# Optimization experiments

Hardware: AMD Instinct MI355X
Metric: run time of the kernel (lower is better)

## Reference

```python
import jax, jax.numpy as jnp
import numpy as np

N, F, E = 10000, 128, 640000
HID_RO = 64


def setup_inputs() -> dict:
    key = jax.random.key(0)
    ks = jax.random.split(key, 16)
    s = 1.0 / np.sqrt(F)
    inp = {
        'h': jax.random.normal(ks[0], (N, F), jnp.float32),
        'src_idx': jax.random.randint(ks[1], (E,), 0, N, jnp.int32),
        'dst_idx': jax.random.randint(ks[2], (E,), 0, N, jnp.int32),
        # message-creation MLP (F -> F -> F)
        'W1': jax.random.normal(ks[3], (F, F), jnp.float32) * s,
        'b1': jnp.zeros((F,), jnp.float32),
        'W2': jax.random.normal(ks[4], (F, F), jnp.float32) * s,
        'b2': jnp.zeros((F,), jnp.float32),
        # attention aggregation kernels
        'node_kernel': jax.random.normal(ks[5], (F, F), jnp.float32) * s,
        'attn_kernel': jax.random.normal(ks[6], (2 * F, 1), jnp.float32) * s,
        # feed-forward update (agg + h -> new h)
        'Wu': jax.random.normal(ks[7], (2 * F, F), jnp.float32) * s,
        'bu': jnp.zeros((F,), jnp.float32),
        # readout MLP (F -> 64 -> 1)
        'Wr1': jax.random.normal(ks[8], (F, HID_RO), jnp.float32) * s,
        'br1': jnp.zeros((HID_RO,), jnp.float32),
        'Wr2': jax.random.normal(ks[9], (HID_RO, 1), jnp.float32) * (1.0 / np.sqrt(HID_RO)),
        'br2': jnp.zeros((1,), jnp.float32),
    }
    return inp


def reference(h, src_idx, dst_idx, W1, b1, W2, b2, node_kernel, attn_kernel,
              Wu, bu, Wr1, br1, Wr2, br2):
    n = h.shape[0]
    # per-edge gather + message-creation NN  [E, F]
    h_src = h[src_idx]
    m = jax.nn.relu(h_src @ W1 + b1) @ W2 + b2
    # attention aggregation (GAT-style): transform messages, score vs dst state
    wh = m @ node_kernel                      # [E, F]
    h_dst = h[dst_idx]                        # [E, F]
    e = jax.nn.leaky_relu(jnp.concatenate([wh, h_dst], axis=-1) @ attn_kernel,
                          negative_slope=0.2)[:, 0]  # [E]
    # per-destination segment softmax (numerically stable)
    e_max = jax.ops.segment_max(e, dst_idx, num_segments=n)
    ex = jnp.exp(e - e_max[dst_idx])
    denom = jax.ops.segment_sum(ex, dst_idx, num_segments=n)
    alpha = ex / (denom[dst_idx] + 1e-9)
    # scatter-reduce weighted messages into destination states  [N, F]
    agg = jax.ops.segment_sum(m * alpha[:, None], dst_idx, num_segments=n)
    # feed-forward update
    h_new = jax.nn.relu(jnp.concatenate([agg, h], axis=-1) @ Wu + bu)
    # readout MLP -> per-node scalar
    out = jax.nn.relu(h_new @ Wr1 + br1) @ Wr2 + br2  # [N, 1]
    return out
```

## Files before the change

### kernel.cpp

```cpp
#include <hip/hip_runtime.h>
#include <hip/hip_bf16.h>
#include <hip/hip_fp16.h>

#define F 128
#define HID 64
#define KMAX 4
#define DEG_CAP 256
#define NTM 16
#define NTU 16
#define CHUNK_LOG 13
#define CHUNK (1 << CHUNK_LOG)


__global__ __launch_bounds__(256) void fused_front(
    const int* __restrict__ dst, unsigned short* __restrict__ cnt,
    unsigned short* __restrict__ rank,
    int e, int n, int histBlocks,
    const float* __restrict__ h,
    const float* __restrict__ W1, const float* __restrict__ b1,
    const float* __restrict__ W2, const float* __restrict__ b2,
    const float* __restrict__ nk, const float* __restrict__ attn,
    __half* __restrict__ Mh, float* __restrict__ p, float* __restrict__ q)
{
    __shared__ __align__(16) int lhist[10240];
    int tid = threadIdx.x;

    if ((int)blockIdx.x < histBlocks) {
        int n4 = n >> 2;
        int4* lh4 = (int4*)lhist;
        for (int i = tid; i < n4; i += 256) lh4[i] = make_int4(0, 0, 0, 0);
        for (int i = (n4 << 2) + tid; i < n; i += 256) lhist[i] = 0;
        __syncthreads();

        int base = (int)blockIdx.x << CHUNK_LOG;
        int lim = min(e - base, CHUNK);
        int lim4 = lim >> 2;
        const int4* d4 = (const int4*)(dst + base);
        for (int k = tid; k < lim4; k += 256) {
            int4 dv = d4[k];
            ushort4 rv;
            rv.x = (unsigned short)atomicAdd(&lhist[dv.x], 1);
            rv.y = (unsigned short)atomicAdd(&lhist[dv.y], 1);
            rv.z = (unsigned short)atomicAdd(&lhist[dv.z], 1);
            rv.w = (unsigned short)atomicAdd(&lhist[dv.w], 1);
            *(ushort4*)&rank[base + 4 * k] = rv;
        }
        for (int k = (lim4 << 2) + tid; k < lim; k += 256)
            rank[base + k] = (unsigned short)atomicAdd(&lhist[dst[base + k]], 1);
        __syncthreads();

        unsigned int* crow = (unsigned int*)(cnt + (size_t)blockIdx.x * n);
        int nh = n >> 1;
        for (int i = tid; i < nh; i += 256) {
            unsigned int v = ((unsigned int)lhist[2 * i] & 0xffffu) |
                             ((unsigned int)lhist[2 * i + 1] << 16);
            crow[i] = v;
        }
        return;
    }

    float (*hsTs)[F] = (float (*)[F])lhist;
    float (*Wc)[F]   = (float (*)[F])((char*)lhist + 8192);
    float* v1s       = (float*)((char*)lhist + 24576);

    int bm = blockIdx.x - histBlocks;
    int row0 = bm * NTM;
    int j0 = (tid & 31) * 4;
    int r0 = (tid >> 5) * 2;

    #pragma unroll
    for (int it = 0; it < 2; ++it) {
        int s4 = tid + it * 256;
        int r = s4 >> 5, c4 = s4 & 31;
        int row = row0 + r;
        float4 v = make_float4(0, 0, 0, 0);
        if (row < n) v = *(const float4*)&h[(size_t)row * F + c4 * 4];
        *(float4*)&hsTs[r][c4 * 4] = v;
    }
    if (tid < F) {
        float a = 0.f;
        const float4* nkr = (const float4*)&nk[(size_t)tid * F];
        const float4* at4 = (const float4*)attn;
        #pragma unroll 8
        for (int j = 0; j < 32; ++j) {
            float4 nv = nkr[j]; float4 av = at4[j];
            a = fmaf(nv.x, av.x, a); a = fmaf(nv.y, av.y, a);
            a = fmaf(nv.z, av.z, a); a = fmaf(nv.w, av.w, a);
        }
        v1s[tid] = a;
    }
    __syncthreads();

    {
        int r = tid >> 4, kp = tid & 15;
        float qa = 0.f;
        #pragma unroll
        for (int c = 0; c < 2; ++c) {
            float4 hv = *(const float4*)&hsTs[r][kp * 8 + c * 4];
            float4 av = *(const float4*)&attn[F + kp * 8 + c * 4];
            qa = fmaf(hv.x, av.x, qa); qa = fmaf(hv.y, av.y, qa);
            qa = fmaf(hv.z, av.z, qa); qa = fmaf(hv.w, av.w, qa);
        }
        #pragma unroll
        for (int off = 1; off < 16; off <<= 1) qa += __shfl_xor(qa, off, 64);
        int row = row0 + r;
        if (kp == 0 && row < n) q[row] = qa;
    }

    float4 acc[2];
    {
        float4 bv = *(const float4*)&b1[j0];
        acc[0] = bv; acc[1] = bv;
    }
    for (int cc = 0; cc < 4; ++cc) {
        int kc = ((cc + bm) & 3) * 32;
        __syncthreads();
        #pragma unroll
        for (int it = 0; it < 4; ++it) {
            int s4 = tid + it * 256;
            int wr = s4 >> 5, wc4 = s4 & 31;
            *(float4*)&Wc[wr][wc4 * 4] =
                *(const float4*)&W1[(size_t)(kc + wr) * F + wc4 * 4];
        }
        __syncthreads();
        #pragma unroll
        for (int k4 = 0; k4 < 8; ++k4) {
            int kk = k4 * 4;
            float4 a0 = *(const float4*)&hsTs[r0 + 0][kc + kk];
            float4 a1 = *(const float4*)&hsTs[r0 + 1][kc + kk];
            #pragma unroll
            for (int k = 0; k < 4; ++k) {
                float4 b = *(const float4*)&Wc[kk + k][j0];
                float av0 = k == 0 ? a0.x : k == 1 ? a0.y : k == 2 ? a0.z : a0.w;
                float av1 = k == 0 ? a1.x : k == 1 ? a1.y : k == 2 ? a1.z : a1.w;
                acc[0].x = fmaf(av0, b.x, acc[0].x); acc[0].y = fmaf(av0, b.y, acc[0].y);
                acc[0].z = fmaf(av0, b.z, acc[0].z); acc[0].w = fmaf(av0, b.w, acc[0].w);
                acc[1].x = fmaf(av1, b.x, acc[1].x); acc[1].y = fmaf(av1, b.y, acc[1].y);
                acc[1].z = fmaf(av1, b.z, acc[1].z); acc[1].w = fmaf(av1, b.w, acc[1].w);
            }
        }
    }
    __syncthreads();
    #pragma unroll
    for (int i = 0; i < 2; ++i) {
        float4 t = acc[i];
        t.x = fmaxf(t.x, 0.f); t.y = fmaxf(t.y, 0.f);
        t.z = fmaxf(t.z, 0.f); t.w = fmaxf(t.w, 0.f);
        *(float4*)&hsTs[r0 + i][j0] = t;
    }

    {
        float4 bv = *(const float4*)&b2[j0];
        acc[0] = bv; acc[1] = bv;
    }
    for (int cc = 0; cc < 4; ++cc) {
        int kc = ((cc + bm) & 3) * 32;
        __syncthreads();
        #pragma unroll
        for (int it = 0; it < 4; ++it) {
            int s4 = tid + it * 256;
            int wr = s4 >> 5, wc4 = s4 & 31;
            *(float4*)&Wc[wr][wc4 * 4] =
                *(const float4*)&W2[(size_t)(kc + wr) * F + wc4 * 4];
        }
        __syncthreads();
        #pragma unroll
        for (int k4 = 0; k4 < 8; ++k4) {
            int kk = k4 * 4;
            float4 a0 = *(const float4*)&hsTs[r0 + 0][kc + kk];
            float4 a1 = *(const float4*)&hsTs[r0 + 1][kc + kk];
            #pragma unroll
            for (int k = 0; k < 4; ++k) {
                float4 b = *(const float4*)&Wc[kk + k][j0];
                float av0 = k == 0 ? a0.x : k == 1 ? a0.y : k == 2 ? a0.z : a0.w;
                float av1 = k == 0 ? a1.x : k == 1 ? a1.y : k == 2 ? a1.z : a1.w;
                acc[0].x = fmaf(av0, b.x, acc[0].x); acc[0].y = fmaf(av0, b.y, acc[0].y);
                acc[0].z = fmaf(av0, b.z, acc[0].z); acc[0].w = fmaf(av0, b.w, acc[0].w);
                acc[1].x = fmaf(av1, b.x, acc[1].x); acc[1].y = fmaf(av1, b.y, acc[1].y);
                acc[1].z = fmaf(av1, b.z, acc[1].z); acc[1].w = fmaf(av1, b.w, acc[1].w);
            }
        }
    }

    float4 v1v = *(const float4*)&v1s[j0];
    #pragma unroll
    for (int i = 0; i < 2; ++i) {
        int row = row0 + r0 + i;
        if (row < n) {
            __half hv[4];
            hv[0] = __float2half(acc[i].x); hv[1] = __float2half(acc[i].y);
            hv[2] = __float2half(acc[i].z); hv[3] = __float2half(acc[i].w);
            *(uint2*)&Mh[(size_t)row * F + j0] = *(uint2*)hv;
        }
        float pp = acc[i].x * v1v.x + acc[i].y * v1v.y +
                   acc[i].z * v1v.z + acc[i].w * v1v.w;
        #pragma unroll
        for (int off = 1; off < 32; off <<= 1) pp += __shfl_xor(pp, off, 64);
        if ((tid & 31) == 0 && row < n) p[row] = pp;
    }
}

__global__ __launch_bounds__(256) void scan_block(
    unsigned short* __restrict__ cnt, int* __restrict__ rstart,
    int* __restrict__ bsum, int n, int hb)
{
    int tid = threadIdx.x;
    int i = blockIdx.x * 256 + tid;
    int run = 0;
    if (i < n) {
        size_t stride = (size_t)n;
        size_t idx = (size_t)i;
        int r = 0;
        for (; r + 8 <= hb; r += 8) {
            int c0 = cnt[idx];
            int c1 = cnt[idx + stride];
            int c2 = cnt[idx + 2 * stride];
            int c3 = cnt[idx + 3 * stride];
            int c4 = cnt[idx + 4 * stride];
            int c5 = cnt[idx + 5 * stride];
            int c6 = cnt[idx + 6 * stride];
            int c7 = cnt[idx + 7 * stride];
            cnt[idx]              = (unsigned short)run;
            cnt[idx + stride]     = (unsigned short)(run + c0);
            cnt[idx + 2 * stride] = (unsigned short)(run + (c0 + c1));
            cnt[idx + 3 * stride] = (unsigned short)(run + (c0 + c1 + c2));
            cnt[idx + 4 * stride] = (unsigned short)(run + (c0 + c1 + c2 + c3));
            cnt[idx + 5 * stride] = (unsigned short)(run + (c0 + c1 + c2 + c3 + c4));
            cnt[idx + 6 * stride] = (unsigned short)(run + (c0 + c1 + c2 + c3 + c4 + c5));
            cnt[idx + 7 * stride] = (unsigned short)(run + (c0 + c1 + c2 + c3 + c4 + c5 + c6));
            run += c0 + c1 + c2 + c3 + c4 + c5 + c6 + c7;
            idx += 8 * stride;
        }
        for (; r < hb; ++r) {
            int c = cnt[idx];
            cnt[idx] = (unsigned short)run;
            run += c;
            idx += stride;
        }
    }
    int v = run;
    int lane = tid & 63, wv = tid >> 6;
    int x = v;
    #pragma unroll
    for (int off = 1; off < 64; off <<= 1) {
        int t = __shfl_up(x, off, 64);
        if (lane >= off) x += t;
    }
    __shared__ int wsum[4];
    if (lane == 63) wsum[wv] = x;
    __syncthreads();
    int woff = 0;
    #pragma unroll
    for (int wdx = 0; wdx < 4; ++wdx) woff += (wdx < wv) ? wsum[wdx] : 0;
    int incl = x + woff;
    if (i < n) rstart[i] = incl - v;
    if (tid == 255) bsum[blockIdx.x] = incl;
}

__global__ __launch_bounds__(256) void fill_kernel(
    const int* __restrict__ dst, const int* __restrict__ src,
    const unsigned short* __restrict__ rank, const int* __restrict__ rstart,
    const unsigned short* __restrict__ cntoff, const int* __restrict__ bsum,
    unsigned short* __restrict__ src_sorted, int n, int nb, int e)
{
    __shared__ int sbo[64];
    int tid = threadIdx.x;
    if (tid < 64) {
        int v = (tid < nb) ? bsum[tid] : 0;
        int x = v;
        #pragma unroll
        for (int off = 1; off < 64; off <<= 1) {
            int t = __shfl_up(x, off, 64);
            if (tid >= off) x += t;
        }
        sbo[tid] = x - v;
    }
    __syncthreads();
    int i = blockIdx.x * 256 + tid;
    if (i < e) {
        int d = dst[i];
        int rep = i >> CHUNK_LOG;
        int pos = rstart[d] + sbo[d >> 8] + (int)cntoff[(size_t)rep * n + d] + (int)rank[i];
        src_sorted[pos] = (unsigned short)src[i];
    }
}

__global__ __launch_bounds__(256) void agg_softmax_gather(
    const __half* __restrict__ Mh, const float* __restrict__ p,
    const float* __restrict__ q, const int* __restrict__ rstart,
    const int* __restrict__ bsum, const unsigned short* __restrict__ src_sorted,
    float* __restrict__ agg, int n, int nb, int e)
{
    __shared__ int2 buf[4][DEG_CAP];
    __shared__ int sbo[64];
    int tid = threadIdx.x;
    if (tid < 64) {
        int v = (tid < nb) ? bsum[tid] : 0;
        int x = v;
        #pragma unroll
        for (int off = 1; off < 64; off <<= 1) {
            int t = __shfl_up(x, off, 64);
            if (tid >= off) x += t;
        }
        sbo[tid] = x - v;
    }
    __syncthreads();

    int lane = tid & 63;
    int wv   = tid >> 6;
    int node = blockIdx.x * 4 + wv;
    if (node >= n) return;

    int start = rstart[node] + sbo[node >> 8];
    int end   = (node + 1 < n) ? rstart[node + 1] + sbo[(node + 1) >> 8] : e;
    int deg   = end - start;
    float qn  = q[node];

    float w[KMAX];
    int   sidx[KMAX];
    float lmax = -1e30f;

    #pragma unroll
    for (int k = 0; k < KMAX; ++k) {
        int i = start + lane + (k << 6);
        bool valid = (i < end);
        int sv = valid ? (int)src_sorted[i] : 0;
        float pv = valid ? p[sv] : 0.0f;
        float sc = pv + qn;
        float ev = (sc > 0.0f) ? sc : 0.2f * sc;
        w[k] = valid ? ev : -1e30f;
        sidx[k] = sv;
        lmax = fmaxf(lmax, w[k]);
    }
    for (int i = start + DEG_CAP + lane; i < end; i += 64) {
        float sc = p[(int)src_sorted[i]] + qn;
        float ev = (sc > 0.0f) ? sc : 0.2f * sc;
        lmax = fmaxf(lmax, ev);
    }
    #pragma unroll
    for (int off = 32; off >= 1; off >>= 1)
        lmax = fmaxf(lmax, __shfl_xor(lmax, off, 64));

    float lsum = 0.0f;
    #pragma unroll
    for (int k = 0; k < KMAX; ++k) {
        float ex = (w[k] > -1e29f) ? __expf(w[k] - lmax) : 0.0f;
        w[k] = ex;
        lsum += ex;
    }
    for (int i = start + DEG_CAP + lane; i < end; i += 64) {
        float sc = p[(int)src_sorted[i]] + qn;
        float ev = (sc > 0.0f) ? sc : 0.2f * sc;
        lsum += __expf(ev - lmax);
    }
    #pragma unroll
    for (int off = 32; off >= 1; off >>= 1)
        lsum += __shfl_xor(lsum, off, 64);
    float inv = 1.0f / (lsum + 1e-9f);

    #pragma unroll
    for (int k = 0; k < KMAX; ++k)
        buf[wv][lane + (k << 6)] = make_int2(__float_as_int(w[k] * inv), sidx[k]);

    const uint4* M16 = (const uint4*)Mh;
    int sub16 = lane & 15;
    int quar  = lane >> 4;
    float acc[8] = {0.f, 0.f, 0.f, 0.f, 0.f, 0.f, 0.f, 0.f};
    int lim = min(deg, DEG_CAP);
    lim = (lim + 15) & ~15;

    for (int base = 0; base < lim; base += 16) {
        int2  rr[4];
        uint4 mm[4];
        #pragma unroll
        for (int u = 0; u < 4; ++u) rr[u] = buf[wv][base + quar + 4 * u];
        #pragma unroll
        for (int u = 0; u < 4; ++u) mm[u] = M16[(size_t)rr[u].y * 16 + sub16];
        #pragma unroll
        for (int u = 0; u < 4; ++u) {
            float wu = __int_as_float(rr[u].x);
            const __half2* hp = (const __half2*)&mm[u];
            float2 f0 = __half22float2(hp[0]);
            float2 f1 = __half22float2(hp[1]);
            float2 f2 = __half22float2(hp[2]);
            float2 f3 = __half22float2(hp[3]);
            acc[0] = fmaf(wu, f0.x, acc[0]); acc[1] = fmaf(wu, f0.y, acc[1]);
            acc[2] = fmaf(wu, f1.x, acc[2]); acc[3] = fmaf(wu, f1.y, acc[3]);
            acc[4] = fmaf(wu, f2.x, acc[4]); acc[5] = fmaf(wu, f2.y, acc[5]);
            acc[6] = fmaf(wu, f3.x, acc[6]); acc[7] = fmaf(wu, f3.y, acc[7]);
        }
    }

    for (int base = start + DEG_CAP; base < end; base += 64) {
        int i = base + lane;
        float ex = 0.f; int sv = 0;
        if (i < end) {
            sv = (int)src_sorted[i];
            float sc = p[sv] + qn;
            float ev = (sc > 0.0f) ? sc : 0.2f * sc;
            ex = __expf(ev - lmax) * inv;
        }
        buf[wv][lane] = make_int2(__float_as_int(ex), sv);
        for (int b2 = 0; b2 < 64; b2 += 4) {
            int2 rr = buf[wv][b2 + quar];
            uint4 mm = M16[(size_t)rr.y * 16 + sub16];
            float wu = __int_as_float(rr.x);
            const __half2* hp = (const __half2*)&mm;
            float2 f0 = __half22float2(hp[0]);
            float2 f1 = __half22float2(hp[1]);
            float2 f2 = __half22float2(hp[2]);
            float2 f3 = __half22float2(hp[3]);
            acc[0] = fmaf(wu, f0.x, acc[0]); acc[1] = fmaf(wu, f0.y, acc[1]);
            acc[2] = fmaf(wu, f1.x, acc[2]); acc[3] = fmaf(wu, f1.y, acc[3]);
            acc[4] = fmaf(wu, f2.x, acc[4]); acc[5] = fmaf(wu, f2.y, acc[5]);
            acc[6] = fmaf(wu, f3.x, acc[6]); acc[7] = fmaf(wu, f3.y, acc[7]);
        }
    }

    #pragma unroll
    for (int j = 0; j < 8; ++j) {
        acc[j] += __shfl_xor(acc[j], 16, 64);
        acc[j] += __shfl_xor(acc[j], 32, 64);
    }
    if (quar == 0) {
        float* dst0 = &agg[(size_t)node * F + sub16 * 8];
        *(float4*)dst0       = make_float4(acc[0], acc[1], acc[2], acc[3]);
        *(float4*)(dst0 + 4) = make_float4(acc[4], acc[5], acc[6], acc[7]);
    }
}

__global__ __launch_bounds__(256) void update_readout_v5(
    const float* __restrict__ agg, const float* __restrict__ h,
    const float* __restrict__ Wu, const float* __restrict__ bu,
    const float* __restrict__ Wr1, const float* __restrict__ br1,
    const float* __restrict__ Wr2, const float* __restrict__ br2,
    float* __restrict__ out, int n)
{
    __shared__ __align__(16) float smem[8192];
    float (*X)[2 * F] = (float (*)[2 * F])smem;
    int tid = threadIdx.x;
    int wv   = tid >> 6;
    int lane = tid & 63;
    int row0 = blockIdx.x * NTU;
    int j0 = (lane & 31) * 4;
    int rh = (lane >> 5) * 8;

    #pragma unroll
    for (int it = 0; it < 4; ++it) {
        int s4 = tid + it * 256;
        int r = s4 >> 6, c4 = s4 & 63;
        int row = row0 + r;
        float4 v = make_float4(0, 0, 0, 0);
        if (row < n) {
            if (c4 < 32) v = *(const float4*)&agg[(size_t)row * F + c4 * 4];
            else         v = *(const float4*)&h[(size_t)row * F + (c4 - 32) * 4];
        }
        *(float4*)&X[r][c4 * 4] = v;
    }
    __syncthreads();

    float4 acc[8];
    #pragma unroll
    for (int i = 0; i < 8; ++i) acc[i] = make_float4(0.f, 0.f, 0.f, 0.f);
    int kbase = wv * 64;
    for (int k4 = 0; k4 < 16; ++k4) {
        int kk = kbase + k4 * 4;
        float4 a[8];
        #pragma unroll
        for (int r = 0; r < 8; ++r) a[r] = *(const float4*)&X[rh + r][kk];
        #pragma unroll
        for (int k = 0; k < 4; ++k) {
            float4 b = *(const float4*)&Wu[(size_t)(kk + k) * F + j0];
            #pragma unroll
            for (int r = 0; r < 8; ++r) {
                float av = k == 0 ? a[r].x : k == 1 ? a[r].y : k == 2 ? a[r].z : a[r].w;
                acc[r].x = fmaf(av, b.x, acc[r].x);
                acc[r].y = fmaf(av, b.y, acc[r].y);
                acc[r].z = fmaf(av, b.z, acc[r].z);
                acc[r].w = fmaf(av, b.w, acc[r].w);
            }
        }
    }
    __syncthreads();

    #pragma unroll
    for (int r = 0; r < 8; ++r)
        *(float4*)&smem[wv * 2048 + (rh + r) * 128 + j0] = acc[r];
    __syncthreads();

    #pragma unroll
    for (int u = 0; u < 2; ++u) {
        int idx = tid * 2 + u;
        int row = idx >> 5, c4 = (idx & 31) * 4;
        float4 s0 = *(const float4*)&smem[0 * 2048 + row * 128 + c4];
        float4 s1 = *(const float4*)&smem[1 * 2048 + row * 128 + c4];
        float4 s2 = *(const float4*)&smem[2 * 2048 + row * 128 + c4];
        float4 s3 = *(const float4*)&smem[3 * 2048 + row * 128 + c4];
        float4 bv = *(const float4*)&bu[c4];
        float4 t;
        t.x = fmaxf(s0.x + s1.x + s2.x + s3.x + bv.x, 0.f);
        t.y = fmaxf(s0.y + s1.y + s2.y + s3.y + bv.y, 0.f);
        t.z = fmaxf(s0.z + s1.z + s2.z + s3.z + bv.z, 0.f);
        t.w = fmaxf(s0.w + s1.w + s2.w + s3.w + bv.w, 0.f);
        *(float4*)&smem[row * 128 + c4] = t;
    }
    __syncthreads();

    int h0 = (lane & 31) * 2;
    float r1a[8], r1b[8];
    #pragma unroll
    for (int r = 0; r < 8; ++r) { r1a[r] = 0.f; r1b[r] = 0.f; }
    int kb2 = wv * 32;
    for (int k4 = 0; k4 < 8; ++k4) {
        int kk = kb2 + k4 * 4;
        float4 a[8];
        #pragma unroll
        for (int r = 0; r < 8; ++r) a[r] = *(const float4*)&smem[(rh + r) * 128 + kk];
        #pragma unroll
        for (int k = 0; k < 4; ++k) {
            float2 b = *(const float2*)&Wr1[(size_t)(kk + k) * HID + h0];
            #pragma unroll
            for (int r = 0; r < 8; ++r) {
                float av = k == 0 ? a[r].x : k == 1 ? a[r].y : k == 2 ? a[r].z : a[r].w;
                r1a[r] = fmaf(av, b.x, r1a[r]);
                r1b[r] = fmaf(av, b.y, r1b[r]);
            }
        }
    }
    #pragma unroll
    for (int r = 0; r < 8; ++r) {
        smem[2048 + wv * 1024 + (rh + r) * 64 + h0]     = r1a[r];
        smem[2048 + wv * 1024 + (rh + r) * 64 + h0 + 1] = r1b[r];
    }
    __syncthreads();

    {
        int row = tid >> 4;
        int hp  = (tid & 15) * 4;
        float val = 0.f;
        #pragma unroll
        for (int j = 0; j < 4; ++j) {
            int hh = hp + j;
            float s = br1[hh]
                    + smem[2048 + 0 * 1024 + row * 64 + hh]
                    + smem[2048 + 1 * 1024 + row * 64 + hh]
                    + smem[2048 + 2 * 1024 + row * 64 + hh]
                    + smem[2048 + 3 * 1024 + row * 64 + hh];
            val = fmaf(fmaxf(s, 0.f), Wr2[hh], val);
        }
        #pragma unroll
        for (int off = 1; off < 16; off <<= 1) val += __shfl_xor(val, off, 64);
        int orow = row0 + row;
        if ((tid & 15) == 0 && orow < n) out[orow] = val + br2[0];
    }
}

extern "C" void kernel_launch(void* const* d_in, const int* in_sizes, int n_in,
                              void* d_out, int out_size, void* d_ws, size_t ws_size,
                              hipStream_t stream) {
    const float* h    = (const float*)d_in[0];
    const int*   src  = (const int*)d_in[1];
    const int*   dst  = (const int*)d_in[2];
    const float* W1   = (const float*)d_in[3];
    const float* b1   = (const float*)d_in[4];
    const float* W2   = (const float*)d_in[5];
    const float* b2   = (const float*)d_in[6];
    const float* nk   = (const float*)d_in[7];
    const float* attn = (const float*)d_in[8];
    const float* Wu   = (const float*)d_in[9];
    const float* bu   = (const float*)d_in[10];
    const float* Wr1  = (const float*)d_in[11];
    const float* br1  = (const float*)d_in[12];
    const float* Wr2  = (const float*)d_in[13];
    const float* br2  = (const float*)d_in[14];
    float* out = (float*)d_out;

    int n = in_sizes[0] / F;
    int e = in_sizes[1];
    int nb = (n + 255) / 256;
    int hb = (e + CHUNK - 1) >> CHUNK_LOG;
    int mlpBlocks  = (n + NTM - 1) / NTM;
    int updBlocks  = (n + NTU - 1) / NTU;
    int fillBlocks = (e + 255) / 256;

    char* ws = (char*)d_ws;
    size_t off = 0;
    auto alloc = [&](size_t bytes) {
        void* pp = ws + off;
        off += (bytes + 511) & ~(size_t)511;
        return pp;
    };
    __half* Mh             = (__half*)alloc((size_t)n * F * 2);
    float* aggws           = (float*)alloc((size_t)n * F * 4);
    float* p               = (float*)alloc((size_t)n * 4);
    float* q               = (float*)alloc((size_t)n * 4);
    unsigned short* cnt    = (unsigned short*)alloc((size_t)hb * n * 2);
    int*   rstart          = (int*)alloc((size_t)(n + 1) * 4);
    int*   bsum            = (int*)alloc((size_t)(nb + 1) * 4);
    unsigned short* rank   = (unsigned short*)alloc((size_t)e * 2);
    unsigned short* srcsort= (unsigned short*)alloc((size_t)e * 2);

    fused_front<<<hb + mlpBlocks, 256, 0, stream>>>(
        dst, cnt, rank, e, n, hb,
        h, W1, b1, W2, b2, nk, attn, Mh, p, q);
    scan_block<<<nb, 256, 0, stream>>>(cnt, rstart, bsum, n, hb);
    fill_kernel<<<fillBlocks, 256, 0, stream>>>(dst, src, rank, rstart,
                                                cnt, bsum, srcsort,
                                                n, nb, e);
    agg_softmax_gather<<<(n + 3) / 4, 256, 0, stream>>>(Mh, p, q, rstart, bsum,
                                                        srcsort, aggws, n, nb, e);
    update_readout_v5<<<updBlocks, 256, 0, stream>>>(aggws, h, Wu, bu,
                                                     Wr1, br1, Wr2, br2,
                                                     out, n);
}
```

Measured before the change: 156.6 us.

## Fuse softmax-gather aggregation into update/readout kernel via shared memory

Merges the per-node softmax aggregation kernel into the update/readout kernel. Each block now handles 16 nodes, with each wave aggregating 4 nodes in turn and writing the result straight into the shared-memory X tile. This removes the global agg buffer round trip and one kernel launch. In exchange the grid shrinks from about 2500 to 625 blocks and each wave processes its nodes serially, which may reduce latency hiding for the gather.

```diff
diff --git a/kernel.cpp b/kernel.cpp
--- a/kernel.cpp
+++ b/kernel.cpp
@@ -285,180 +285,174 @@
     }
 }
 
-__global__ __launch_bounds__(256) void agg_softmax_gather(
+__global__ __launch_bounds__(256) void agg_update(
     const __half* __restrict__ Mh, const float* __restrict__ p,
     const float* __restrict__ q, const int* __restrict__ rstart,
     const int* __restrict__ bsum, const unsigned short* __restrict__ src_sorted,
-    float* __restrict__ agg, int n, int nb, int e)
-{
-    __shared__ int2 buf[4][DEG_CAP];
-    __shared__ int sbo[64];
-    int tid = threadIdx.x;
-    if (tid < 64) {
-        int v = (tid < nb) ? bsum[tid] : 0;
-        int x = v;
-        #pragma unroll
-        for (int off = 1; off < 64; off <<= 1) {
-            int t = __shfl_up(x, off, 64);
-            if (tid >= off) x += t;
-        }
-        sbo[tid] = x - v;
-    }
-    __syncthreads();
-
-    int lane = tid & 63;
-    int wv   = tid >> 6;
-    int node = blockIdx.x * 4 + wv;
-    if (node >= n) return;
-
-    int start = rstart[node] + sbo[node >> 8];
-    int end   = (node + 1 < n) ? rstart[node + 1] + sbo[(node + 1) >> 8] : e;
-    int deg   = end - start;
-    float qn  = q[node];
-
-    float w[KMAX];
-    int   sidx[KMAX];
-    float lmax = -1e30f;
-
-    #pragma unroll
-    for (int k = 0; k < KMAX; ++k) {
-        int i = start + lane + (k << 6);
-        bool valid = (i < end);
-        int sv = valid ? (int)src_sorted[i] : 0;
-        float pv = valid ? p[sv] : 0.0f;
-        float sc = pv + qn;
-        float ev = (sc > 0.0f) ? sc : 0.2f * sc;
-        w[k] = valid ? ev : -1e30f;
-        sidx[k] = sv;
-        lmax = fmaxf(lmax, w[k]);
-    }
-    for (int i = start + DEG_CAP + lane; i < end; i += 64) {
-        float sc = p[(int)src_sorted[i]] + qn;
-        float ev = (sc > 0.0f) ? sc : 0.2f * sc;
-        lmax = fmaxf(lmax, ev);
-    }
-    #pragma unroll
-    for (int off = 32; off >= 1; off >>= 1)
-        lmax = fmaxf(lmax, __shfl_xor(lmax, off, 64));
-
-    float lsum = 0.0f;
-    #pragma unroll
-    for (int k = 0; k < KMAX; ++k) {
-        float ex = (w[k] > -1e29f) ? __expf(w[k] - lmax) : 0.0f;
-        w[k] = ex;
-        lsum += ex;
-    }
-    for (int i = start + DEG_CAP + lane; i < end; i += 64) {
-        float sc = p[(int)src_sorted[i]] + qn;
-        float ev = (sc > 0.0f) ? sc : 0.2f * sc;
-        lsum += __expf(ev - lmax);
-    }
-    #pragma unroll
-    for (int off = 32; off >= 1; off >>= 1)
-        lsum += __shfl_xor(lsum, off, 64);
-    float inv = 1.0f / (lsum + 1e-9f);
-
-    #pragma unroll
-    for (int k = 0; k < KMAX; ++k)
-        buf[wv][lane + (k << 6)] = make_int2(__float_as_int(w[k] * inv), sidx[k]);
-
-    const uint4* M16 = (const uint4*)Mh;
-    int sub16 = lane & 15;
-    int quar  = lane >> 4;
-    float acc[8] = {0.f, 0.f, 0.f, 0.f, 0.f, 0.f, 0.f, 0.f};
-    int lim = min(deg, DEG_CAP);
-    lim = (lim + 15) & ~15;
-
-    for (int base = 0; base < lim; base += 16) {
-        int2  rr[4];
-        uint4 mm[4];
-        #pragma unroll
-        for (int u = 0; u < 4; ++u) rr[u] = buf[wv][base + quar + 4 * u];
-        #pragma unroll
-        for (int u = 0; u < 4; ++u) mm[u] = M16[(size_t)rr[u].y * 16 + sub16];
-        #pragma unroll
-        for (int u = 0; u < 4; ++u) {
-            float wu = __int_as_float(rr[u].x);
-            const __half2* hp = (const __half2*)&mm[u];
-            float2 f0 = __half22float2(hp[0]);
-            float2 f1 = __half22float2(hp[1]);
-            float2 f2 = __half22float2(hp[2]);
-            float2 f3 = __half22float2(hp[3]);
-            acc[0] = fmaf(wu, f0.x, acc[0]); acc[1] = fmaf(wu, f0.y, acc[1]);
-            acc[2] = fmaf(wu, f1.x, acc[2]); acc[3] = fmaf(wu, f1.y, acc[3]);
-            acc[4] = fmaf(wu, f2.x, acc[4]); acc[5] = fmaf(wu, f2.y, acc[5]);
-            acc[6] = fmaf(wu, f3.x, acc[6]); acc[7] = fmaf(wu, f3.y, acc[7]);
-        }
-    }
-
-    for (int base = start + DEG_CAP; base < end; base += 64) {
-        int i = base + lane;
-        float ex = 0.f; int sv = 0;
-        if (i < end) {
-            sv = (int)src_sorted[i];
-            float sc = p[sv] + qn;
-            float ev = (sc > 0.0f) ? sc : 0.2f * sc;
-            ex = __expf(ev - lmax) * inv;
-        }
-        buf[wv][lane] = make_int2(__float_as_int(ex), sv);
-        for (int b2 = 0; b2 < 64; b2 += 4) {
-            int2 rr = buf[wv][b2 + quar];
-            uint4 mm = M16[(size_t)rr.y * 16 + sub16];
-            float wu = __int_as_float(rr.x);
-            const __half2* hp = (const __half2*)&mm;
-            float2 f0 = __half22float2(hp[0]);
-            float2 f1 = __half22float2(hp[1]);
-            float2 f2 = __half22float2(hp[2]);
-            float2 f3 = __half22float2(hp[3]);
-            acc[0] = fmaf(wu, f0.x, acc[0]); acc[1] = fmaf(wu, f0.y, acc[1]);
-            acc[2] = fmaf(wu, f1.x, acc[2]); acc[3] = fmaf(wu, f1.y, acc[3]);
-            acc[4] = fmaf(wu, f2.x, acc[4]); acc[5] = fmaf(wu, f2.y, acc[5]);
-            acc[6] = fmaf(wu, f3.x, acc[6]); acc[7] = fmaf(wu, f3.y, acc[7]);
-        }
-    }
-
-    #pragma unroll
-    for (int j = 0; j < 8; ++j) {
-        acc[j] += __shfl_xor(acc[j], 16, 64);
-        acc[j] += __shfl_xor(acc[j], 32, 64);
-    }
-    if (quar == 0) {
-        float* dst0 = &agg[(size_t)node * F + sub16 * 8];
-        *(float4*)dst0       = make_float4(acc[0], acc[1], acc[2], acc[3]);
-        *(float4*)(dst0 + 4) = make_float4(acc[4], acc[5], acc[6], acc[7]);
-    }
-}
-
-__global__ __launch_bounds__(256) void update_readout_v5(
-    const float* __restrict__ agg, const float* __restrict__ h,
+    const float* __restrict__ h,
     const float* __restrict__ Wu, const float* __restrict__ bu,
     const float* __restrict__ Wr1, const float* __restrict__ br1,
     const float* __restrict__ Wr2, const float* __restrict__ br2,
-    float* __restrict__ out, int n)
+    float* __restrict__ out, int n, int nb, int e)
 {
     __shared__ __align__(16) float smem[8192];
     float (*X)[2 * F] = (float (*)[2 * F])smem;
+    int2* bufa = (int2*)&smem[4096];
+    int*  sbo  = (int*)&smem[6144];
+
     int tid = threadIdx.x;
     int wv   = tid >> 6;
     int lane = tid & 63;
     int row0 = blockIdx.x * NTU;
+
+    if (tid < 64) {
+        int v = (tid < nb) ? bsum[tid] : 0;
+        int x = v;
+        #pragma unroll
+        for (int off = 1; off < 64; off <<= 1) {
+            int t = __shfl_up(x, off, 64);
+            if (tid >= off) x += t;
+        }
+        sbo[tid] = x - v;
+    }
+    #pragma unroll
+    for (int it = 0; it < 2; ++it) {
+        int s4 = tid + it * 256;
+        int r = s4 >> 5, c4 = s4 & 31;
+        int row = row0 + r;
+        float4 v = make_float4(0, 0, 0, 0);
+        if (row < n) v = *(const float4*)&h[(size_t)row * F + c4 * 4];
+        *(float4*)&X[r][128 + c4 * 4] = v;
+    }
+    __syncthreads();
+
+    const uint4* M16 = (const uint4*)Mh;
+    int sub16 = lane & 15;
+    int quar  = lane >> 4;
+    int2* bufw = bufa + wv * DEG_CAP;
+
+    for (int s = 0; s < 4; ++s) {
+        int lr = wv * 4 + s;
+        int node = row0 + lr;
+        if (node >= n) break;
+
+        int start = rstart[node] + sbo[node >> 8];
+        int end   = (node + 1 < n) ? rstart[node + 1] + sbo[(node + 1) >> 8] : e;
+        int deg   = end - start;
+        float qn  = q[node];
+
+        float w[KMAX];
+        int   sidx[KMAX];
+        float lmax = -1e30f;
+
+        #pragma unroll
+        for (int k = 0; k < KMAX; ++k) {
+            int i = start + lane + (k << 6);
+            bool valid = (i < end);
+            int sv = valid ? (int)src_sorted[i] : 0;
+            float pv = valid ? p[sv] : 0.0f;
+            float sc = pv + qn;
+            float ev = (sc > 0.0f) ? sc : 0.2f * sc;
+            w[k] = valid ? ev : -1e30f;
+            sidx[k] = sv;
+            lmax = fmaxf(lmax, w[k]);
+        }
+        for (int i = start + DEG_CAP + lane; i < end; i += 64) {
+            float sc = p[(int)src_sorted[i]] + qn;
+            float ev = (sc > 0.0f) ? sc : 0.2f * sc;
+            lmax = fmaxf(lmax, ev);
+        }
+        #pragma unroll
+        for (int off = 32; off >= 1; off >>= 1)
+            lmax = fmaxf(lmax, __shfl_xor(lmax, off, 64));
+
+        float lsum = 0.0f;
+        #pragma unroll
+        for (int k = 0; k < KMAX; ++k) {
+            float ex = (w[k] > -1e29f) ? __expf(w[k] - lmax) : 0.0f;
+            w[k] = ex;
+            lsum += ex;
+        }
+        for (int i = start + DEG_CAP + lane; i < end; i += 64) {
+            float sc = p[(int)src_sorted[i]] + qn;
+            float ev = (sc > 0.0f) ? sc : 0.2f * sc;
+            lsum += __expf(ev - lmax);
+        }
+        #pragma unroll
+        for (int off = 32; off >= 1; off >>= 1)
+            lsum += __shfl_xor(lsum, off, 64);
+        float inv = 1.0f / (lsum + 1e-9f);
+
+        #pragma unroll
+        for (int k = 0; k < KMAX; ++k)
+            bufw[lane + (k << 6)] = make_int2(__float_as_int(w[k] * inv), sidx[k]);
+
+        float acc[8] = {0.f, 0.f, 0.f, 0.f, 0.f, 0.f, 0.f, 0.f};
+        int lim = min(deg, DEG_CAP);
+        lim = (lim + 15) & ~15;
+
+        for (int base = 0; base < lim; base += 16) {
+            int2  rr[4];
+            uint4 mm[4];
+            #pragma unroll
+            for (int u = 0; u < 4; ++u) rr[u] = bufw[base + quar + 4 * u];
+            #pragma unroll
+            for (int u = 0; u < 4; ++u) mm[u] = M16[(size_t)rr[u].y * 16 + sub16];
+            #pragma unroll
+            for (int u = 0; u < 4; ++u) {
+                float wu = __int_as_float(rr[u].x);
+                const __half2* hp = (const __half2*)&mm[u];
+                float2 f0 = __half22float2(hp[0]);
+                float2 f1 = __half22float2(hp[1]);
+                float2 f2 = __half22float2(hp[2]);
+                float2 f3 = __half22float2(hp[3]);
+                acc[0] = fmaf(wu, f0.x, acc[0]); acc[1] = fmaf(wu, f0.y, acc[1]);
+                acc[2] = fmaf(wu, f1.x, acc[2]); acc[3] = fmaf(wu, f1.y, acc[3]);
+                acc[4] = fmaf(wu, f2.x, acc[4]); acc[5] = fmaf(wu, f2.y, acc[5]);
+                acc[6] = fmaf(wu, f3.x, acc[6]); acc[7] = fmaf(wu, f3.y, acc[7]);
+            }
+        }
+
+        for (int base = start + DEG_CAP; base < end; base += 64) {
+            int i = base + lane;
+            float ex = 0.f; int sv = 0;
+            if (i < end) {
+                sv = (int)src_sorted[i];
+                float sc = p[sv] + qn;
+                float ev = (sc > 0.0f) ? sc : 0.2f * sc;
+                ex = __expf(ev - lmax) * inv;
+            }
+            bufw[lane] = make_int2(__float_as_int(ex), sv);
+            for (int b2 = 0; b2 < 64; b2 += 4) {
+                int2 rr = bufw[b2 + quar];
+                uint4 mm = M16[(size_t)rr.y * 16 + sub16];
+                float wu = __int_as_float(rr.x);
+                const __half2* hp = (const __half2*)&mm;
+                float2 f0 = __half22float2(hp[0]);
+                float2 f1 = __half22float2(hp[1]);
+                float2 f2 = __half22float2(hp[2]);
+                float2 f3 = __half22float2(hp[3]);
+                acc[0] = fmaf(wu, f0.x, acc[0]); acc[1] = fmaf(wu, f0.y, acc[1]);
+                acc[2] = fmaf(wu, f1.x, acc[2]); acc[3] = fmaf(wu, f1.y, acc[3]);
+                acc[4] = fmaf(wu, f2.x, acc[4]); acc[5] = fmaf(wu, f2.y, acc[5]);
+                acc[6] = fmaf(wu, f3.x, acc[6]); acc[7] = fmaf(wu, f3.y, acc[7]);
+            }
+        }
+
+        #pragma unroll
+        for (int j = 0; j < 8; ++j) {
+            acc[j] += __shfl_xor(acc[j], 16, 64);
+            acc[j] += __shfl_xor(acc[j], 32, 64);
+        }
+        if (quar == 0) {
+            *(float4*)&X[lr][sub16 * 8]     = make_float4(acc[0], acc[1], acc[2], acc[3]);
+            *(float4*)&X[lr][sub16 * 8 + 4] = make_float4(acc[4], acc[5], acc[6], acc[7]);
+        }
+    }
+    __syncthreads();
+
     int j0 = (lane & 31) * 4;
     int rh = (lane >> 5) * 8;
-
-    #pragma unroll
-    for (int it = 0; it < 4; ++it) {
-        int s4 = tid + it * 256;
-        int r = s4 >> 6, c4 = s4 & 63;
-        int row = row0 + r;
-        float4 v = make_float4(0, 0, 0, 0);
-        if (row < n) {
-            if (c4 < 32) v = *(const float4*)&agg[(size_t)row * F + c4 * 4];
-            else         v = *(const float4*)&h[(size_t)row * F + (c4 - 32) * 4];
-        }
-        *(float4*)&X[r][c4 * 4] = v;
-    }
-    __syncthreads();
-
     float4 acc[8];
     #pragma unroll
     for (int i = 0; i < 8; ++i) acc[i] = make_float4(0.f, 0.f, 0.f, 0.f);
@@ -580,7 +574,7 @@
     int nb = (n + 255) / 256;
     int hb = (e + CHUNK - 1) >> CHUNK_LOG;
     int mlpBlocks  = (n + NTM - 1) / NTM;
-    int updBlocks  = (n + NTU - 1) / NTU;
+    int fusBlocks  = (n + NTU - 1) / NTU;
     int fillBlocks = (e + 255) / 256;
 
     char* ws = (char*)d_ws;
@@ -591,7 +585,6 @@
         return pp;
     };
     __half* Mh             = (__half*)alloc((size_t)n * F * 2);
-    float* aggws           = (float*)alloc((size_t)n * F * 4);
     float* p               = (float*)alloc((size_t)n * 4);
     float* q               = (float*)alloc((size_t)n * 4);
     unsigned short* cnt    = (unsigned short*)alloc((size_t)hb * n * 2);
@@ -607,9 +600,7 @@
     fill_kernel<<<fillBlocks, 256, 0, stream>>>(dst, src, rank, rstart,
                                                 cnt, bsum, srcsort,
                                                 n, nb, e);
-    agg_softmax_gather<<<(n + 3) / 4, 256, 0, stream>>>(Mh, p, q, rstart, bsum,
-                                                        srcsort, aggws, n, nb, e);
-    update_readout_v5<<<updBlocks, 256, 0, stream>>>(aggws, h, Wu, bu,
-                                                     Wr1, br1, Wr2, br2,
-                                                     out, n);
+    agg_update<<<fusBlocks, 256, 0, stream>>>(Mh, p, q, rstart, bsum, srcsort,
+                                              h, Wu, bu, Wr1, br1, Wr2, br2,
+                                              out, n, nb, e);
 }
```

Result: no change. 157.3 us (+0.4%).
